# Performance work log

Hardware: AMD Instinct MI355X
Metric: run time of the kernel (lower is better)

## Reference

```python
import jax, jax.numpy as jnp
import numpy as np

B, S, IN, OUT = 4, 32, 8192, 8192


def setup_inputs() -> dict:
    key = jax.random.key(0)
    k1, k2, k3, k4 = jax.random.split(key, 4)
    x = jax.random.normal(k1, (B, S, IN), dtype=jnp.float32)
    # FP8-e4m3 stored weight: round-trip through fp8 so values are representable,
    # then keep as fp32 (the module upcasts to fp32 before the matmul anyway).
    w = jax.random.normal(k2, (OUT, IN), dtype=jnp.float32)
    weight = w.astype(jnp.float8_e4m3fn).astype(jnp.float32)
    # per-output-channel scale, strictly positive small values
    weight_scale = jax.random.uniform(k3, (OUT, 1), dtype=jnp.float32,
                                      minval=1e-3, maxval=2e-2)
    bias = (jax.random.normal(k4, (OUT,), dtype=jnp.float32) * 0.01).astype(jnp.float16)
    return {"x": x, "weight": weight, "weight_scale": weight_scale, "bias": bias}


def reference(x, weight, weight_scale, bias):
    # dequantize fp8 weight to fp32 with per-channel scale  [OUT, IN]
    dq_w = weight * weight_scale
    # x @ dq_w.T  -> [B, S, OUT]
    out = jnp.einsum("bsi,oi->bso", x.astype(jnp.float32), dq_w)
    out = out + bias.astype(jnp.float32)
    return out
```

## Files before the change

kernel.cpp:

```cpp
#include <hip/hip_runtime.h>
#include <hip/hip_bf16.h>
#include <hip/hip_fp16.h>


namespace {
constexpr int MM = 128;
constexpr int NN = 8192;
constexpr int KK = 8192;
constexpr int KSPLIT = 4;
constexpr int KPB = KK / KSPLIT;
constexpr int KT = 128;
constexpr int NCH = KPB / KT;
constexpr int NKS = KPB / 32;
constexpr int LDSX = KT + 8;

typedef __attribute__((ext_vector_type(8))) short bf16x8;
typedef __attribute__((ext_vector_type(4))) float f32x4;

__device__ __forceinline__ bf16x8 pack8(float4 a, float4 b) {
    union { __hip_bfloat16 h[8]; bf16x8 v; } p;
    p.h[0] = __float2bfloat16(a.x); p.h[1] = __float2bfloat16(a.y);
    p.h[2] = __float2bfloat16(a.z); p.h[3] = __float2bfloat16(a.w);
    p.h[4] = __float2bfloat16(b.x); p.h[5] = __float2bfloat16(b.y);
    p.h[6] = __float2bfloat16(b.z); p.h[7] = __float2bfloat16(b.w);
    return p.v;
}
}

__global__ __launch_bounds__(256, 2)
void cfp8_gemm_nws(const float* __restrict__ x, const float* __restrict__ w,
                   const float* __restrict__ c1, const float* __restrict__ c2,
                   float* __restrict__ out)
{
    __shared__ __align__(16) __hip_bfloat16 lx[2][MM * LDSX];
    __shared__ int s_c1s, s_kind;

    const int tid  = threadIdx.x;
    const int lane = tid & 63;
    const int wid  = tid >> 6;
    const int l16  = lane & 15;
    const int quad = lane >> 4;
    const int kz   = blockIdx.y;
    const int n0   = blockIdx.x * 64 + wid * 16;
    const size_t kbase = (size_t)kz * KPB;

    if (tid < 64) {
        float v = c1[tid * 64];
        unsigned long long b = __ballot((v > 1e-4f) && (v < 0.5f));
        int c1s = (b == ~0ull) ? 1 : 0;
        const void* bp = c1s ? (const void*)c2 : (const void*)c1;
        float vf = __half2float(((const __half*)bp)[tid * 64]);
        unsigned long long bf_ = __ballot((vf < 0.5f) && (vf > -0.5f));
        float vb = __bfloat162float(((const __hip_bfloat16*)bp)[tid * 64]);
        unsigned long long bb = __ballot((vb < 0.5f) && (vb > -0.5f));
        if (tid == 0) {
            s_c1s  = c1s;
            s_kind = (bf_ == ~0ull) ? 0 : ((bb == ~0ull) ? 1 : 2);
        }
    }
    __syncthreads();
    const float* scalep = s_c1s ? c1 : c2;
    const void*  biasp  = s_c1s ? (const void*)c2 : (const void*)c1;
    const float sc = scalep[n0 + l16];
    float bs = 0.0f;
    if (kz == 0) {
        if (s_kind == 0)      bs = __half2float(((const __half*)biasp)[n0 + l16]);
        else if (s_kind == 1) bs = __bfloat162float(((const __hip_bfloat16*)biasp)[n0 + l16]);
        else                  bs = ((const float*)biasp)[n0 + l16];
    }

    const int srow = tid >> 1;
    const int shf  = tid & 1;
    const float* xrow = x + (size_t)srow * KK + kbase + shf * 64;

    const float* wlane = w + (size_t)(n0 + l16) * KK + kbase + quad * 8;

    float4 sr[16];
#pragma unroll
    for (int i = 0; i < 16; ++i) sr[i] = *(const float4*)(xrow + i * 4);

    float4 wa = *(const float4*)(wlane);
    float4 wb = *(const float4*)(wlane + 4);

#pragma unroll
    for (int j = 0; j < 8; ++j) {
        bf16x8 v = pack8(sr[2 * j], sr[2 * j + 1]);
        *(bf16x8*)&lx[0][srow * LDSX + shf * 64 + j * 8] = v;
    }
    __syncthreads();

    f32x4 acc[8];
#pragma unroll
    for (int t = 0; t < 8; ++t) acc[t] = (f32x4){0.f, 0.f, 0.f, 0.f};

    for (int c = 0; c < NCH; ++c) {
        const int buf = c & 1;

        if (c + 1 < NCH) {
#pragma unroll
            for (int i = 0; i < 16; ++i)
                sr[i] = *(const float4*)(xrow + (c + 1) * KT + i * 4);
        }
        __builtin_amdgcn_sched_barrier(0);

#pragma unroll
        for (int s = 0; s < 4; ++s) {
            const int ksn = (c * 4 + s + 1 < NKS) ? (c * 4 + s + 1) : (NKS - 1);
            const float* wn = wlane + (size_t)ksn * 32;
            float4 na = *(const float4*)(wn);
            float4 nb = *(const float4*)(wn + 4);

            bf16x8 bfrag = pack8(wa, wb);
            bf16x8 af[8];
#pragma unroll
            for (int t = 0; t < 8; ++t)
                af[t] = *(const bf16x8*)&lx[buf][(t * 16 + l16) * LDSX + s * 32 + quad * 8];
#pragma unroll
            for (int t = 0; t < 8; ++t)
                acc[t] = __builtin_amdgcn_mfma_f32_16x16x32_bf16(af[t], bfrag, acc[t], 0, 0, 0);

            wa = na; wb = nb;
        }

        if (c + 1 < NCH) {
#pragma unroll
            for (int j = 0; j < 8; ++j) {
                bf16x8 v = pack8(sr[2 * j], sr[2 * j + 1]);
                *(bf16x8*)&lx[buf ^ 1][srow * LDSX + shf * 64 + j * 8] = v;
            }
            __syncthreads();
        }
    }

#pragma unroll
    for (int t = 0; t < 8; ++t) {
#pragma unroll
        for (int r = 0; r < 4; ++r) {
            atomicAdd(out + (size_t)(t * 16 + quad * 4 + r) * NN + n0 + l16,
                      acc[t][r] * sc + bs);
        }
    }
}

extern "C" void kernel_launch(void* const* d_in, const int* in_sizes, int n_in,
                              void* d_out, int out_size, void* d_ws, size_t ws_size,
                              hipStream_t stream) {
    int iw = 0;
    for (int i = 1; i < n_in; ++i) if (in_sizes[i] > in_sizes[iw]) iw = i;
    int ix = -1;
    for (int i = 0; i < n_in; ++i)
        if (i != iw && (ix < 0 || in_sizes[i] > in_sizes[ix])) ix = i;
    const float* c1 = nullptr;
    const float* c2 = nullptr;
    for (int i = 0; i < n_in; ++i) {
        if (i == iw || i == ix) continue;
        if (!c1) c1 = (const float*)d_in[i];
        else     c2 = (const float*)d_in[i];
    }
    const float* w = (const float*)d_in[iw];
    const float* x = (const float*)d_in[ix];
    float* out = (float*)d_out;

    (void)d_ws; (void)ws_size;

    hipMemsetAsync(d_out, 0, (size_t)out_size * sizeof(float), stream);
    cfp8_gemm_nws<<<dim3(NN / 64, KSPLIT), dim3(256), 0, stream>>>(x, w, c1, c2, out);
}
```

Baseline: 432.7 us.

## Stage fp32 tiles via direct global-to-LDS loads with swizzle, 128x128 block tiles

Replaces the register-staged x load and per-lane direct weight loads with async global_load_lds transfers of both x and weight fp32 tiles into XOR-swizzled double-buffered LDS. Each block now computes a 128x128 output tile with a 2x2 wave layout and a 4x4 MFMA grid per wave. The bf16 conversion moves to fragment-load time. The intent is to cut register pressure and VMEM issue overhead and to raise reuse per LDS fragment. In exchange, LDS grows to 128 KB per block, which allows only one block per CU, and the grid has half as many blocks (256), which may underfill the GPU.

```diff
diff --git a/kernel.cpp b/kernel.cpp
--- a/kernel.cpp
+++ b/kernel.cpp
@@ -4,15 +4,12 @@
 
 
 namespace {
-constexpr int MM = 128;
 constexpr int NN = 8192;
 constexpr int KK = 8192;
 constexpr int KSPLIT = 4;
 constexpr int KPB = KK / KSPLIT;
-constexpr int KT = 128;
-constexpr int NCH = KPB / KT;
-constexpr int NKS = KPB / 32;
-constexpr int LDSX = KT + 8;
+constexpr int BK  = 64;
+constexpr int NIT = KPB / BK;
 
 typedef __attribute__((ext_vector_type(8))) short bf16x8;
 typedef __attribute__((ext_vector_type(4))) float f32x4;
@@ -25,14 +22,22 @@
     p.h[6] = __float2bfloat16(b.z); p.h[7] = __float2bfloat16(b.w);
     return p.v;
 }
+
+__device__ __forceinline__ void gload_lds16(const void* g, void* l) {
+    __builtin_amdgcn_global_load_lds(
+        (const __attribute__((address_space(1))) unsigned int*)g,
+        (__attribute__((address_space(3))) unsigned int*)l,
+        16, 0, 0);
+}
 }
 
-__global__ __launch_bounds__(256, 2)
-void cfp8_gemm_nws(const float* __restrict__ x, const float* __restrict__ w,
+__global__ __launch_bounds__(256, 1)
+void cfp8_gemm_r10(const float* __restrict__ x, const float* __restrict__ w,
                    const float* __restrict__ c1, const float* __restrict__ c2,
                    float* __restrict__ out)
 {
-    __shared__ __align__(16) __hip_bfloat16 lx[2][MM * LDSX];
+    __shared__ __align__(16) float ldsA[2][128 * BK];
+    __shared__ __align__(16) float ldsB[2][128 * BK];
     __shared__ int s_c1s, s_kind;
 
     const int tid  = threadIdx.x;
@@ -40,8 +45,10 @@
     const int wid  = tid >> 6;
     const int l16  = lane & 15;
     const int quad = lane >> 4;
+    const int wr   = wid >> 1;
+    const int wc   = wid & 1;
+    const int nb0  = blockIdx.x * 128;
     const int kz   = blockIdx.y;
-    const int n0   = blockIdx.x * 64 + wid * 16;
     const size_t kbase = (size_t)kz * KPB;
 
     if (tid < 64) {
@@ -58,86 +65,95 @@
             s_kind = (bf_ == ~0ull) ? 0 : ((bb == ~0ull) ? 1 : 2);
         }
     }
+
+    unsigned off[8];
+#pragma unroll
+    for (int j = 0; j < 8; ++j) {
+        const int q   = (wid * 8 + j) * 64 + lane;
+        const int row = q >> 4;
+        const int c16 = q & 15;
+        const int swz = c16 ^ (row & 7);
+        off[j] = (unsigned)row * (KK * 4) + (unsigned)swz * 16;
+    }
+    const char* xsrc = (const char*)(x + kbase);
+    const char* wsrc = (const char*)(w + (size_t)nb0 * KK + kbase);
+
+#define STAGE(buf_, c_)                                                        \
+    {                                                                          \
+        const size_t kb_ = (size_t)(c_) * (BK * 4);                            \
+        _Pragma("unroll")                                                      \
+        for (int j = 0; j < 8; ++j) {                                          \
+            gload_lds16(xsrc + kb_ + off[j],                                   \
+                        (char*)&ldsA[buf_][0] + (wid * 8 + j) * 1024);         \
+            gload_lds16(wsrc + kb_ + off[j],                                   \
+                        (char*)&ldsB[buf_][0] + (wid * 8 + j) * 1024);         \
+        }                                                                      \
+    }
+
+#define LOADFRAG(dst_, lds_, rb_, s_)                                          \
+    {                                                                          \
+        const int row_ = (rb_) + l16;                                          \
+        const int cx_  = (s_) * 8 + quad * 2;                                  \
+        const int sw_  = row_ & 7;                                             \
+        float4 a0_ = *(const float4*)&(lds_)[(row_ * 16 + (cx_ ^ sw_)) * 4];   \
+        float4 a1_ = *(const float4*)&(lds_)[(row_ * 16 + ((cx_ + 1) ^ sw_)) * 4]; \
+        dst_ = pack8(a0_, a1_);                                                \
+    }
+
+    f32x4 acc[4][4];
+#pragma unroll
+    for (int i = 0; i < 4; ++i)
+#pragma unroll
+        for (int j = 0; j < 4; ++j) acc[i][j] = (f32x4){0.f, 0.f, 0.f, 0.f};
+
+    STAGE(0, 0)
     __syncthreads();
+
+    for (int c = 0; c < NIT; ++c) {
+        const int buf = c & 1;
+        if (c + 1 < NIT) STAGE(buf ^ 1, c + 1)
+
+#pragma unroll
+        for (int s = 0; s < 2; ++s) {
+            bf16x8 af[4], bfr[4];
+#pragma unroll
+            for (int i = 0; i < 4; ++i)
+                LOADFRAG(af[i], ldsA[buf], wr * 64 + i * 16, s)
+#pragma unroll
+            for (int j = 0; j < 4; ++j)
+                LOADFRAG(bfr[j], ldsB[buf], wc * 64 + j * 16, s)
+#pragma unroll
+            for (int i = 0; i < 4; ++i)
+#pragma unroll
+                for (int j = 0; j < 4; ++j)
+                    acc[i][j] = __builtin_amdgcn_mfma_f32_16x16x32_bf16(
+                        af[i], bfr[j], acc[i][j], 0, 0, 0);
+        }
+
+        if (c + 1 < NIT) __syncthreads();
+    }
+#undef STAGE
+#undef LOADFRAG
+
     const float* scalep = s_c1s ? c1 : c2;
     const void*  biasp  = s_c1s ? (const void*)c2 : (const void*)c1;
-    const float sc = scalep[n0 + l16];
-    float bs = 0.0f;
-    if (kz == 0) {
-        if (s_kind == 0)      bs = __half2float(((const __half*)biasp)[n0 + l16]);
-        else if (s_kind == 1) bs = __bfloat162float(((const __hip_bfloat16*)biasp)[n0 + l16]);
-        else                  bs = ((const float*)biasp)[n0 + l16];
-    }
-
-    const int srow = tid >> 1;
-    const int shf  = tid & 1;
-    const float* xrow = x + (size_t)srow * KK + kbase + shf * 64;
-
-    const float* wlane = w + (size_t)(n0 + l16) * KK + kbase + quad * 8;
-
-    float4 sr[16];
 #pragma unroll
-    for (int i = 0; i < 16; ++i) sr[i] = *(const float4*)(xrow + i * 4);
-
-    float4 wa = *(const float4*)(wlane);
-    float4 wb = *(const float4*)(wlane + 4);
-
+    for (int j = 0; j < 4; ++j) {
+        const int col = nb0 + wc * 64 + j * 16 + l16;
+        const float scj = scalep[col];
+        float bsj = 0.0f;
+        if (kz == 0) {
+            if (s_kind == 0)      bsj = __half2float(((const __half*)biasp)[col]);
+            else if (s_kind == 1) bsj = __bfloat162float(((const __hip_bfloat16*)biasp)[col]);
+            else                  bsj = ((const float*)biasp)[col];
+        }
 #pragma unroll
-    for (int j = 0; j < 8; ++j) {
-        bf16x8 v = pack8(sr[2 * j], sr[2 * j + 1]);
-        *(bf16x8*)&lx[0][srow * LDSX + shf * 64 + j * 8] = v;
-    }
-    __syncthreads();
-
-    f32x4 acc[8];
+        for (int i = 0; i < 4; ++i) {
+            const int rb = wr * 64 + i * 16 + quad * 4;
 #pragma unroll
-    for (int t = 0; t < 8; ++t) acc[t] = (f32x4){0.f, 0.f, 0.f, 0.f};
-
-    for (int c = 0; c < NCH; ++c) {
-        const int buf = c & 1;
-
-        if (c + 1 < NCH) {
-#pragma unroll
-            for (int i = 0; i < 16; ++i)
-                sr[i] = *(const float4*)(xrow + (c + 1) * KT + i * 4);
-        }
-        __builtin_amdgcn_sched_barrier(0);
-
-#pragma unroll
-        for (int s = 0; s < 4; ++s) {
-            const int ksn = (c * 4 + s + 1 < NKS) ? (c * 4 + s + 1) : (NKS - 1);
-            const float* wn = wlane + (size_t)ksn * 32;
-            float4 na = *(const float4*)(wn);
-            float4 nb = *(const float4*)(wn + 4);
-
-            bf16x8 bfrag = pack8(wa, wb);
-            bf16x8 af[8];
-#pragma unroll
-            for (int t = 0; t < 8; ++t)
-                af[t] = *(const bf16x8*)&lx[buf][(t * 16 + l16) * LDSX + s * 32 + quad * 8];
-#pragma unroll
-            for (int t = 0; t < 8; ++t)
-                acc[t] = __builtin_amdgcn_mfma_f32_16x16x32_bf16(af[t], bfrag, acc[t], 0, 0, 0);
-
-            wa = na; wb = nb;
-        }
-
-        if (c + 1 < NCH) {
-#pragma unroll
-            for (int j = 0; j < 8; ++j) {
-                bf16x8 v = pack8(sr[2 * j], sr[2 * j + 1]);
-                *(bf16x8*)&lx[buf ^ 1][srow * LDSX + shf * 64 + j * 8] = v;
-            }
-            __syncthreads();
-        }
-    }
-
-#pragma unroll
-    for (int t = 0; t < 8; ++t) {
-#pragma unroll
-        for (int r = 0; r < 4; ++r) {
-            atomicAdd(out + (size_t)(t * 16 + quad * 4 + r) * NN + n0 + l16,
-                      acc[t][r] * sc + bs);
+            for (int r = 0; r < 4; ++r)
+                atomicAdd(out + (size_t)(rb + r) * NN + col,
+                          acc[i][j][r] * scj + bsj);
         }
     }
 }
@@ -164,5 +180,5 @@
     (void)d_ws; (void)ws_size;
 
     hipMemsetAsync(d_out, 0, (size_t)out_size * sizeof(float), stream);
-    cfp8_gemm_nws<<<dim3(NN / 64, KSPLIT), dim3(256), 0, stream>>>(x, w, c1, c2, out);
+    cfp8_gemm_r10<<<dim3(NN / 128, KSPLIT), dim3(256), 0, stream>>>(x, w, c1, c2, out);
 }
```

Result: faster. 401.0 us (-7.3%).
